# Kernel tuning notes

Measured on AMD Instinct MI355X. Metric: run time of the kernel, lower is better.

## Reference

```python
import jax, jax.numpy as jnp
import numpy as np

ALPHA = 0.2
N_NODES = 50000
N_REL = 500
E = 500000
E_NHOP = 100000


def l2norm(v):
    n = jnp.sqrt(jnp.sum(v * v, axis=1, keepdims=True))
    return v / jnp.maximum(n, 1e-12)


def sp_attention(x, src, dst, edge_embed, a, a2, concat):
    # a: [out, 2*din + drel]; edge_m = a @ cat(x[src], x[dst], edge_embed).T, done blockwise
    N, din = x.shape
    a_src, a_dst, a_rel = a[:, :din], a[:, din:2 * din], a[:, 2 * din:]
    edge_m = x[src] @ a_src.T + x[dst] @ a_dst.T + edge_embed @ a_rel.T  # [E, out]
    powers = -jax.nn.leaky_relu(edge_m @ a2, ALPHA)                      # [E]
    edge_e = jnp.exp(powers)
    e_rowsum = jax.ops.segment_sum(edge_e, src, num_segments=N)
    e_rowsum = jnp.where(e_rowsum == 0.0, 1e-12, e_rowsum)
    h_prime = jax.ops.segment_sum(edge_e[:, None] * edge_m, src, num_segments=N)
    h_prime = h_prime / e_rowsum[:, None]
    return jax.nn.elu(h_prime) if concat else h_prime


def spgat(x, rel, src, dst, edge_type, et_nhop, head_params, W, out_a, out_a2):
    ee = jnp.concatenate([rel[edge_type], rel[et_nhop[:, 0]] + rel[et_nhop[:, 1]]], axis=0)
    x = jnp.concatenate([sp_attention(x, src, dst, ee, a, a2, True) for a, a2 in head_params], axis=1)
    out_rel = rel @ W
    ee2 = jnp.concatenate([out_rel[edge_type], out_rel[et_nhop[:, 0]] + out_rel[et_nhop[:, 1]]], axis=0)
    x = jax.nn.elu(sp_attention(x, src, dst, ee2, out_a, out_a2, False))
    return x, out_rel


def forward_impl(entity_emb, relation_emb, W_entities,
                 g0_a0, g0_s0, g0_a1, g0_s1, g0_W, g0_oa, g0_os,
                 g1_a0, g1_s0, g1_W, g1_oa, g1_os,
                 edge_list, edge_type, train_indices_nhop, batch_inputs):
    ent = l2norm(entity_emb)
    rel = l2norm(relation_emb)
    # n-hop edges: (col3 -> col0), relation pair in cols 1,2
    src = jnp.concatenate([edge_list[0], train_indices_nhop[:, 3]])
    dst = jnp.concatenate([edge_list[1], train_indices_nhop[:, 0]])
    et_nhop = train_indices_nhop[:, 1:3]
    mask = jnp.zeros((ent.shape[0],), ent.dtype).at[batch_inputs[:, 2]].set(1.0)
    # layer 0 (2 heads)
    ent_up = ent @ W_entities
    rel_up = rel @ W_entities
    e_new, r_new = spgat(ent, rel, src, dst, edge_type, et_nhop,
                         [(g0_a0, g0_s0), (g0_a1, g0_s1)], g0_W, g0_oa, g0_os)
    ent = l2norm(ent_up + mask[:, None] * e_new)
    rel = l2norm(rel_up + r_new)
    # layer 1 (1 head, residual)
    e_new, r_new = spgat(ent, rel, src, dst, edge_type, et_nhop,
                         [(g1_a0, g1_s0)], g1_W, g1_oa, g1_os)
    ent = l2norm(ent + mask[:, None] * e_new)
    rel = l2norm(rel + r_new)
    return ent, rel


def setup_inputs() -> dict:
    key = jax.random.key(0)
    ks = jax.random.split(key, 20)
    s = 0.05
    inp = {
        "entity_emb": jax.random.normal(ks[0], (N_NODES, 100), jnp.float32),
        "relation_emb": jax.random.normal(ks[1], (N_REL, 100), jnp.float32),
        "W_entities": jax.random.normal(ks[2], (100, 200), jnp.float32) * s,
        "g0_a0": jax.random.normal(ks[3], (100, 300), jnp.float32) * s,
        "g0_s0": jax.random.normal(ks[4], (100,), jnp.float32) * s,
        "g0_a1": jax.random.normal(ks[5], (100, 300), jnp.float32) * s,
        "g0_s1": jax.random.normal(ks[6], (100,), jnp.float32) * s,
        "g0_W": jax.random.normal(ks[7], (100, 200), jnp.float32) * s,
        "g0_oa": jax.random.normal(ks[8], (200, 600), jnp.float32) * s,
        "g0_os": jax.random.normal(ks[9], (200,), jnp.float32) * s,
        "g1_a0": jax.random.normal(ks[10], (200, 600), jnp.float32) * s,
        "g1_s0": jax.random.normal(ks[11], (200,), jnp.float32) * s,
        "g1_W": jax.random.normal(ks[12], (200, 200), jnp.float32) * s,
        "g1_oa": jax.random.normal(ks[13], (200, 600), jnp.float32) * s,
        "g1_os": jax.random.normal(ks[14], (200,), jnp.float32) * s,
        "edge_list": jax.random.randint(ks[15], (2, E), 0, N_NODES, jnp.int64 if jax.config.jax_enable_x64 else jnp.int32),
        "edge_type": jax.random.randint(ks[16], (E,), 0, N_REL),
        "train_indices_nhop": jax.random.randint(ks[17], (E_NHOP, 4), 0, N_REL),
        "batch_inputs": jax.random.randint(ks[18], (10000, 3), 0, N_NODES),
    }
    return inp


def reference(entity_emb, relation_emb, W_entities,
              g0_a0, g0_s0, g0_a1, g0_s1, g0_W, g0_oa, g0_os,
              g1_a0, g1_s0, g1_W, g1_oa, g1_os,
              edge_list, edge_type, train_indices_nhop, batch_inputs):
    return forward_impl(entity_emb, relation_emb, W_entities,
                        g0_a0, g0_s0, g0_a1, g0_s1, g0_W, g0_oa, g0_os,
                        g1_a0, g1_s0, g1_W, g1_oa, g1_os,
                        edge_list, edge_type, train_indices_nhop, batch_inputs)
```

## Files before the change

kernel.cpp:

```cpp
#include <hip/hip_runtime.h>
#include <hip/hip_bf16.h>
#include <cstdint>
#include <cstddef>

#define NNODES 50000
#define NRELS  500
#define NEDGE  500000
#define NETOT  600000
#define MP     50048
#define RPAD   512
#define HOTN   512

typedef __attribute__((ext_vector_type(8))) short bf16x8;
typedef __attribute__((ext_vector_type(4))) float f32x4;

__device__ inline float bf2f(unsigned short s){
  union { unsigned u; float f; } v; v.u = ((unsigned)s) << 16; return v.f;
}
__device__ inline unsigned short f2bf(float f){
  __hip_bfloat16 h = __float2bfloat16(f);
  return __builtin_bit_cast(unsigned short, h);
}

struct WEnt { int src, ld, boff, rows, K, tr, dstoff, Kp, rp; };
// ... 94 lines not shown

__global__ void k_mask_set(const int* __restrict__ batch, float* __restrict__ mask, int nb){
  int i = blockIdx.x*blockDim.x + threadIdx.x;
  if (i < nb) mask[batch[3*i+2]] = 1.0f;
}

__global__ void k_hist(const int* __restrict__ el, const int* __restrict__ nh, int* __restrict__ deg){
  int e = blockIdx.x*blockDim.x + threadIdx.x;
  if (e >= NETOT) return;
  int s = (e < NEDGE) ? el[e] : nh[4*(e-NEDGE)+3];
  atomicAdd(&deg[s], 1);
}
__global__ void k_scan1(int* __restrict__ data, int n, int* __restrict__ part){
  __shared__ int sh[256];
  int t = threadIdx.x, i = blockIdx.x*256 + t;
  int v = (i < n) ? data[i] : 0;
  sh[t] = v; __syncthreads();
  for (int o = 1; o < 256; o <<= 1){
    int x = (t >= o) ? sh[t-o] : 0;
    __syncthreads(); sh[t] += x; __syncthreads();
  }
  if (i < n) data[i] = sh[t] - v;
  if (t == 255) part[blockIdx.x] = sh[255];
}
__global__ void k_scan2(int* __restrict__ part, int nb){
  __shared__ int sh[256];
  int t = threadIdx.x;
  int v = (t < nb) ? part[t] : 0;
  sh[t] = v; __syncthreads();
  for (int o = 1; o < 256; o <<= 1){
    int x = (t >= o) ? sh[t-o] : 0;
    __syncthreads(); sh[t] += x; __syncthreads();
  }
  if (t < nb) part[t] = sh[t] - v;
}
__global__ void k_scan3(int* __restrict__ data, int n, const int* __restrict__ part){
  int i = blockIdx.x*256 + threadIdx.x;
  if (i < n) data[i] += part[blockIdx.x];
  if (i == 0) data[n] = NETOT;
}
__global__ void k_scatter(const int* __restrict__ el, const int* __restrict__ et,
                          const int* __restrict__ nh, const int* __restrict__ rowofs,
                          int* __restrict__ cur, int4* __restrict__ erec){
  int e = blockIdx.x*blockDim.x + threadIdx.x;
  if (e >= NETOT) return;
  int s, d, t0, t1;
  if (e < NEDGE){ s = el[e]; d = el[NEDGE+e]; t0 = et[e]; t1 = NRELS; }
  else { int i = e - NEDGE; s = nh[4*i+3]; d = nh[4*i+0]; t0 = nh[4*i+1]; t1 = nh[4*i+2]; }
  int p = rowofs[s] + atomicAdd(&cur[s], 1);
  erec[p] = make_int4(d, t0, t1, 0);
}

template<bool FINAL>
__global__ __launch_bounds__(64) void k_combine2(
    const __hip_bfloat16* __restrict__ baseE, const __hip_bfloat16* __restrict__ hE,
    const float* __restrict__ mask,
    const __hip_bfloat16* __restrict__ baseR, const __hip_bfloat16* __restrict__ hR,
    float* __restrict__ outfE, float* __restrict__ outfR,
    __hip_bfloat16* __restrict__ outbE, __hip_bfloat16* __restrict__ outbR)
{
  int n = blockIdx.x, lane = threadIdx.x;
  bool isE = n < NNODES;
  int row = isE ? n : n - NNODES;
  const __hip_bfloat16* b = (isE ? baseE : baseR) + (size_t)row*224;
  const __hip_bfloat16* h = (isE ? hE : hR) + (size_t)row*224;
  float m = isE ? mask[row] : 1.0f;
  int c = lane*4;
  float4 v = make_float4(0.f,0.f,0.f,0.f);
  if (c < 200){
    ushort4 bb = *(const ushort4*)(b + c);
    ushort4 hh = *(const ushort4*)(h + c);
    v.x = bf2f(bb.x) + m*bf2f(hh.x);
    v.y = bf2f(bb.y) + m*bf2f(hh.y);
    v.z = bf2f(bb.z) + m*bf2f(hh.z);
    v.w = bf2f(bb.w) + m*bf2f(hh.w);
  }
  float ss = v.x*v.x + v.y*v.y + v.z*v.z + v.w*v.w;
  #pragma unroll
  for (int o = 32; o; o >>= 1) ss += __shfl_xor(ss, o, 64);
  float sc = 1.0f / fmaxf(sqrtf(ss), 1e-12f);
  if constexpr (FINAL){
    if (c < 200){
      float* o = (isE ? outfE : outfR) + (size_t)row*200 + c;
      *(float4*)o = make_float4(v.x*sc, v.y*sc, v.z*sc, v.w*sc);
    }
  } else {
    if (c < 224){
      __hip_bfloat16* o = (isE ? outbE : outbR) + (size_t)row*224 + c;
      ushort4 w4; w4.x = f2bf(v.x*sc); w4.y = f2bf(v.y*sc); w4.z = f2bf(v.z*sc); w4.w = f2bf(v.w*sc);
      *(ushort4*)o = w4;
    }
  }
}

__global__ __launch_bounds__(256) void k_rowdot3(
    const __hip_bfloat16* __restrict__ XN, const float* __restrict__ wtN, int GN,
    float* __restrict__ n0, float* __restrict__ n1, float* __restrict__ n2, float* __restrict__ n3,
    const __hip_bfloat16* __restrict__ XR, const float* __restrict__ wtR, int GR,
    float* __restrict__ r0, float* __restrict__ r1)
{
  int wave = threadIdx.x >> 6, lane = threadIdx.x & 63;
  int b = blockIdx.x;
  if (b < 12500){
    int row = b*4 + wave;
    const __hip_bfloat16* xr = XN + (size_t)row*512 + lane*8;
    const float* wr = wtN + lane*8;
    float p = 0.f;
    #pragma unroll
    for (int k = 0; k < 2; k++){
      ushort4 x = *(const ushort4*)(xr + 4*k);
      float4 a = *(const float4*)(wr + 4*k);
      p += bf2f(x.x)*a.x + bf2f(x.y)*a.y + bf2f(x.z)*a.z + bf2f(x.w)*a.w;
    }
    for (int o = GN>>1; o; o >>= 1) p += __shfl_xor(p, o, 64);
    if ((lane & (GN-1)) == 0){
      int g = lane / GN;
      float* out = (g==0)?n0:(g==1)?n1:(g==2)?n2:n3;
      out[row] = p;
    }
  } else {
    int row = (b - 12500)*4 + wave;
    if (row >= NRELS + 1) return;
    const __hip_bfloat16* xr = XR + (size_t)row*256 + lane*4;
    ushort4 x = *(const ushort4*)xr;
    float4 a = *(const float4*)(wtR + lane*4);
    float p = bf2f(x.x)*a.x + bf2f(x.y)*a.y + bf2f(x.z)*a.z + bf2f(x.w)*a.w;
    for (int o = GR>>1; o; o >>= 1) p += __shfl_xor(p, o, 64);
    if ((lane & (GR-1)) == 0){
      int g = lane / GR;
      float* out = (g==0)?r0:r1;
      out[row] = p;
    }
  }
}

struct GemmDesc {
  const __hip_bfloat16 *A, *B; __hip_bfloat16* C;
  int M, Nn, Kp, ldc, gx, nblk;
};
__global__ __launch_bounds__(256) void k_gemm2(GemmDesc g1, GemmDesc g2)
{
  __shared__ __hip_bfloat16 As[128*32];
  __shared__ __hip_bfloat16 Bs[64*32];
// ... 23 lines not shown

  for (int kk = 0; kk < Kp; kk += 32){
    {
      int p0 = ap ^ ((ar0 >> 1) & 3);
      const char* s0 = Ab + ((size_t)(m0 + ar0)*Kp + kk)*2 + p0*16;
      __builtin_amdgcn_global_load_lds((const __attribute__((address_space(1))) void*)s0,
          (__attribute__((address_space(3))) void*)(asB + wave*1024), 16, 0, 0);
      int p1 = ap ^ ((ar1 >> 1) & 3);
      const char* s1 = Ab + ((size_t)(m0 + ar1)*Kp + kk)*2 + p1*16;
      __builtin_amdgcn_global_load_lds((const __attribute__((address_space(1))) void*)s1,
          (__attribute__((address_space(3))) void*)(asB + 4096 + wave*1024), 16, 0, 0);
      int pb = ap ^ ((ar0 >> 1) & 3);
      const char* sb = Bb + ((size_t)(n0 + ar0)*Kp + kk)*2 + pb*16;
      __builtin_amdgcn_global_load_lds((const __attribute__((address_space(1))) void*)sb,
          (__attribute__((address_space(3))) void*)(bsB + wave*1024), 16, 0, 0);
    }
    __syncthreads();
    bf16x8 av[4], bv[2];
    #pragma unroll
    for (int mf = 0; mf < 4; mf++){
      int row = wr*64 + mf*16 + li;
      int p = lg ^ ((row >> 1) & 3);
      av[mf] = *(const bf16x8*)(asB + row*64 + p*16);
    }
    #pragma unroll
    for (int nf = 0; nf < 2; nf++){
      int row = wc*32 + nf*16 + li;
      int p = lg ^ ((row >> 1) & 3);
      bv[nf] = *(const bf16x8*)(bsB + row*64 + p*16);
    }
    #pragma unroll
    for (int mf = 0; mf < 4; mf++)
      #pragma unroll
      for (int nf = 0; nf < 2; nf++)
        acc[mf][nf] = __builtin_amdgcn_mfma_f32_16x16x32_bf16(av[mf], bv[nf], acc[mf][nf], 0, 0, 0);
    __syncthreads();
  }
  #pragma unroll
  for (int mf = 0; mf < 4; mf++){
    #pragma unroll
    for (int nf = 0; nf < 2; nf++){
      int gc = n0 + wc*32 + nf*16 + li;
      if (gc >= g.Nn) continue;
      int gr0 = m0 + wr*64 + mf*16 + lg*4;
      #pragma unroll
      for (int rr = 0; rr < 4; rr++){
        int gr = gr0 + rr;
        if (gr < g.M) g.C[(size_t)gr*g.ldc + gc] = __float2bfloat16(acc[mf][nf][rr]);
      }
    }
  }
}

__device__ inline void agg5_edges(int bstart, int end, int bstep,
    const int4* __restrict__ erec, float psn,
    const float* __restrict__ pd, const float* __restrict__ prs,
    const __hip_bfloat16* __restrict__ XSD, int ldx, int cxd,
    const __hip_bfloat16* __restrict__ RRb, int ldr, int crr,
    int lane, float& Sl, float4& accO)
{
  bool act = lane < 50;
  const __hip_bfloat16* xb = XSD + cxd + 4*lane;
  const __hip_bfloat16* rb = RRb + crr + 4*lane;
  float4 accA = make_float4(0.f,0.f,0.f,0.f);
  float4 accB = make_float4(0.f,0.f,0.f,0.f);
  for (int b = bstart; b < end; b += bstep){
    int j = b + lane;
    int4 e = make_int4(0, NRELS, NRELS, 0);
    float wv = 0.f;
    if (j < end){
      e = erec[j];
      float lg = psn + pd[e.x] + prs[e.y] + prs[e.z];
      wv = __expf(-((lg > 0.f) ? lg : 0.2f*lg));
    }
    Sl += wv;
    int m = end - b; if (m > 64) m = 64;
    int i = 0;
    for (; i + 1 < m; i += 2){
      float wA = __shfl(wv, i),   wB = __shfl(wv, i+1);
      int dA = __shfl(e.x, i),   tA0 = __shfl(e.y, i),   tA1 = __shfl(e.z, i);
      int dB = __shfl(e.x, i+1), tB0 = __shfl(e.y, i+1), tB1 = __shfl(e.z, i+1);
      if (act){
        ushort4 xA = *(const ushort4*)(xb + (size_t)dA*ldx);
        ushort4 rA = *(const ushort4*)(rb + (size_t)tA0*ldr);
        ushort4 xB = *(const ushort4*)(xb + (size_t)dB*ldx);
        ushort4 rB = *(const ushort4*)(rb + (size_t)tB0*ldr);
        float ax = bf2f(xA.x)+bf2f(rA.x), ay = bf2f(xA.y)+bf2f(rA.y);
        float az = bf2f(xA.z)+bf2f(rA.z), aw = bf2f(xA.w)+bf2f(rA.w);
        if (tA1 != NRELS){
          ushort4 rc = *(const ushort4*)(rb + (size_t)tA1*ldr);
          ax += bf2f(rc.x); ay += bf2f(rc.y); az += bf2f(rc.z); aw += bf2f(rc.w);
        }
        float bx = bf2f(xB.x)+bf2f(rB.x), by = bf2f(xB.y)+bf2f(rB.y);
        float bz = bf2f(xB.z)+bf2f(rB.z), bw = bf2f(xB.w)+bf2f(rB.w);
        if (tB1 != NRELS){
          ushort4 rc = *(const ushort4*)(rb + (size_t)tB1*ldr);
          bx += bf2f(rc.x); by += bf2f(rc.y); bz += bf2f(rc.z); bw += bf2f(rc.w);
        }
        accA.x += wA*ax; accA.y += wA*ay; accA.z += wA*az; accA.w += wA*aw;
        accB.x += wB*bx; accB.y += wB*by; accB.z += wB*bz; accB.w += wB*bw;
      }
    }
    if (i < m){
      float wA = __shfl(wv, i);
      int dA = __shfl(e.x, i), tA0 = __shfl(e.y, i), tA1 = __shfl(e.z, i);
      if (act){
        ushort4 xA = *(const ushort4*)(xb + (size_t)dA*ldx);
        ushort4 rA = *(const ushort4*)(rb + (size_t)tA0*ldr);
        float ax = bf2f(xA.x)+bf2f(rA.x), ay = bf2f(xA.y)+bf2f(rA.y);
        float az = bf2f(xA.z)+bf2f(rA.z), aw = bf2f(xA.w)+bf2f(rA.w);
        if (tA1 != NRELS){
          ushort4 rc = *(const ushort4*)(rb + (size_t)tA1*ldr);
          ax += bf2f(rc.x); ay += bf2f(rc.y); az += bf2f(rc.z); aw += bf2f(rc.w);
        }
        accA.x += wA*ax; accA.y += wA*ay; accA.z += wA*az; accA.w += wA*aw;
      }
    }
  }
  accO.x += accA.x + accB.x; accO.y += accA.y + accB.y;
  accO.z += accA.z + accB.z; accO.w += accA.w + accB.w;
}

__device__ inline void agg5_finalize(int n, float S, float4 acc, int lane,
    const __hip_bfloat16* __restrict__ XSD, int ldx, int cxs,
    __hip_bfloat16* __restrict__ outb, int ldb, int coffb)
{
  if (lane >= 50) return;
  float inv = (S > 0.f) ? 1.0f/S : 0.f;
  ushort4 xs4 = *(const ushort4*)(XSD + (size_t)n*ldx + cxs + 4*lane);
  float h0 = (S > 0.f) ? bf2f(xs4.x) + acc.x*inv : 0.f;
  float h1 = (S > 0.f) ? bf2f(xs4.y) + acc.y*inv : 0.f;
  float h2 = (S > 0.f) ? bf2f(xs4.z) + acc.z*inv : 0.f;
  float h3 = (S > 0.f) ? bf2f(xs4.w) + acc.w*inv : 0.f;
  h0 = (h0 > 0.f) ? h0 : expm1f(h0);
  h1 = (h1 > 0.f) ? h1 : expm1f(h1);
  h2 = (h2 > 0.f) ? h2 : expm1f(h2);
  h3 = (h3 > 0.f) ? h3 : expm1f(h3);
  ushort4 o; o.x = f2bf(h0); o.y = f2bf(h1); o.z = f2bf(h2); o.w = f2bf(h3);
  *(ushort4*)(outb + (size_t)n*ldb + coffb + 4*lane) = o;
}

__global__ __launch_bounds__(256) void k_agg5(
    const int* __restrict__ rowofs, const int4* __restrict__ erec,
    const float* __restrict__ ps, const float* __restrict__ pd, const float* __restrict__ prs,
    const __hip_bfloat16* __restrict__ XSD,
    const __hip_bfloat16* __restrict__ RRb,
    __hip_bfloat16* __restrict__ outb, int ldb, int coffb)
{
  __shared__ float4 redA[256];
  __shared__ float redS[4];
  int bid = blockIdx.x;
  int wave = threadIdx.x >> 6, lane = threadIdx.x & 63;

  if (bid < HOTN){
    int n = bid;
    int beg = rowofs[n], end = rowofs[n+1];
    float psn = ps[n];
    float Sl = 0.f;
    float4 acc = make_float4(0.f,0.f,0.f,0.f);
    agg5_edges(beg + wave*64, end, 256, erec, psn, pd, prs,
               XSD, 512, 256, RRb, 256, 0, lane, Sl, acc);
    float Sw = Sl;
    #pragma unroll
    for (int o = 32; o; o >>= 1) Sw += __shfl_xor(Sw, o, 64);
    redA[threadIdx.x] = acc;
    if (lane == 0) redS[wave] = Sw;
    __syncthreads();
    if (wave == 0){
      float4 a0 = redA[lane], a1 = redA[lane+64], a2 = redA[lane+128], a3 = redA[lane+192];
      float4 at = make_float4(a0.x+a1.x+a2.x+a3.x, a0.y+a1.y+a2.y+a3.y,
                              a0.z+a1.z+a2.z+a3.z, a0.w+a1.w+a2.w+a3.w);
      float St = redS[0] + redS[1] + redS[2] + redS[3];
      agg5_finalize(n, St, at, lane, XSD, 512, 0, outb, ldb, coffb);
    }
  } else {
    int n = HOTN + (bid - HOTN)*4 + wave;
    int beg = rowofs[n], end = rowofs[n+1];
    float psn = ps[n];
    float Sl = 0.f;
    float4 acc = make_float4(0.f,0.f,0.f,0.f);
    agg5_edges(beg, end, 64, erec, psn, pd, prs,
               XSD, 512, 256, RRb, 256, 0, lane, Sl, acc);
    float S = Sl;
    #pragma unroll
    for (int o = 32; o; o >>= 1) S += __shfl_xor(S, o, 64);
    agg5_finalize(n, S, acc, lane, XSD, 512, 0, outb, ldb, coffb);
  }
}

__device__ inline void aggh_edges(int bstart, int end, int bstep,
    const int4* __restrict__ erec,
    float ps0n, const float* __restrict__ pd0, const float* __restrict__ prs0,
    float ps1n, const float* __restrict__ pd1, const float* __restrict__ prs1,
    const __hip_bfloat16* __restrict__ XSD, int ldx,
    const __hip_bfloat16* __restrict__ RRb, int ldr,
    int lane, float& Sl0, float& Sl1, float4& accO)
{
  bool act = lane < 50;
  int head = (lane >= 25) ? 1 : 0;
  int li = lane - 25*head;
  const __hip_bfloat16* xb = XSD + (head ? 384 : 128) + 4*li;
  const __hip_bfloat16* rb = RRb + (head ? 128 : 0) + 4*li;
  float4 accA = make_float4(0.f,0.f,0.f,0.f);
  float4 accB = make_float4(0.f,0.f,0.f,0.f);
  for (int b = bstart; b < end; b += bstep){
    int j = b + lane;
    int4 e = make_int4(0, NRELS, NRELS, 0);
    float wv0 = 0.f, wv1 = 0.f;
    if (j < end){
      e = erec[j];
      float lg0 = ps0n + pd0[e.x] + prs0[e.y] + prs0[e.z];
      float lg1 = ps1n + pd1[e.x] + prs1[e.y] + prs1[e.z];
      wv0 = __expf(-((lg0 > 0.f) ? lg0 : 0.2f*lg0));
      wv1 = __expf(-((lg1 > 0.f) ? lg1 : 0.2f*lg1));
    }
    Sl0 += wv0; Sl1 += wv1;
    int m = end - b; if (m > 64) m = 64;
    int i = 0;
    for (; i + 1 < m; i += 2){
      float wA0 = __shfl(wv0, i),   wA1 = __shfl(wv1, i);
      float wB0 = __shfl(wv0, i+1), wB1 = __shfl(wv1, i+1);
      int dA = __shfl(e.x, i),   tA0 = __shfl(e.y, i),   tA1 = __shfl(e.z, i);
      int dB = __shfl(e.x, i+1), tB0 = __shfl(e.y, i+1), tB1 = __shfl(e.z, i+1);
      if (act){
        float wA = head ? wA1 : wA0;
        float wB = head ? wB1 : wB0;
        ushort4 xA = *(const ushort4*)(xb + (size_t)dA*ldx);
        ushort4 rA = *(const ushort4*)(rb + (size_t)tA0*ldr);
        ushort4 xB = *(const ushort4*)(xb + (size_t)dB*ldx);
        ushort4 rB = *(const ushort4*)(rb + (size_t)tB0*ldr);
        float ax = bf2f(xA.x)+bf2f(rA.x), ay = bf2f(xA.y)+bf2f(rA.y);
        float az = bf2f(xA.z)+bf2f(rA.z), aw = bf2f(xA.w)+bf2f(rA.w);
        if (tA1 != NRELS){
          ushort4 rc = *(const ushort4*)(rb + (size_t)tA1*ldr);
          ax += bf2f(rc.x); ay += bf2f(rc.y); az += bf2f(rc.z); aw += bf2f(rc.w);
        }
        float bx = bf2f(xB.x)+bf2f(rB.x), by = bf2f(xB.y)+bf2f(rB.y);
        float bz = bf2f(xB.z)+bf2f(rB.z), bw = bf2f(xB.w)+bf2f(rB.w);
        if (tB1 != NRELS){
          ushort4 rc = *(const ushort4*)(rb + (size_t)tB1*ldr);
          bx += bf2f(rc.x); by += bf2f(rc.y); bz += bf2f(rc.z); bw += bf2f(rc.w);
        }
        accA.x += wA*ax; accA.y += wA*ay; accA.z += wA*az; accA.w += wA*aw;
        accB.x += wB*bx; accB.y += wB*by; accB.z += wB*bz; accB.w += wB*bw;
      }
    }
    if (i < m){
      float wA0 = __shfl(wv0, i), wA1 = __shfl(wv1, i);
      int dA = __shfl(e.x, i), tA0 = __shfl(e.y, i), tA1 = __shfl(e.z, i);
      if (act){
        float wA = head ? wA1 : wA0;
        ushort4 xA = *(const ushort4*)(xb + (size_t)dA*ldx);
        ushort4 rA = *(const ushort4*)(rb + (size_t)tA0*ldr);
        float ax = bf2f(xA.x)+bf2f(rA.x), ay = bf2f(xA.y)+bf2f(rA.y);
        float az = bf2f(xA.z)+bf2f(rA.z), aw = bf2f(xA.w)+bf2f(rA.w);
        if (tA1 != NRELS){
          ushort4 rc = *(const ushort4*)(rb + (size_t)tA1*ldr);
          ax += bf2f(rc.x); ay += bf2f(rc.y); az += bf2f(rc.z); aw += bf2f(rc.w);
        }
        accA.x += wA*ax; accA.y += wA*ay; accA.z += wA*az; accA.w += wA*aw;
      }
    }
  }
  accO.x += accA.x + accB.x; accO.y += accA.y + accB.y;
  accO.z += accA.z + accB.z; accO.w += accA.w + accB.w;
}

__device__ inline void aggh_finalize(int n, float S0, float S1, float4 acc, int lane,
    const __hip_bfloat16* __restrict__ XSD,
    __hip_bfloat16* __restrict__ outb, int ldb)
{
  if (lane >= 50) return;
  int head = (lane >= 25) ? 1 : 0;
  int li = lane - 25*head;
  float S = head ? S1 : S0;
  float inv = (S > 0.f) ? 1.0f/S : 0.f;
  ushort4 xs4 = *(const ushort4*)(XSD + (size_t)n*512 + (head ? 256 : 0) + 4*li);
  float h0 = (S > 0.f) ? bf2f(xs4.x) + acc.x*inv : 0.f;
  float h1 = (S > 0.f) ? bf2f(xs4.y) + acc.y*inv : 0.f;
  float h2 = (S > 0.f) ? bf2f(xs4.z) + acc.z*inv : 0.f;
  float h3 = (S > 0.f) ? bf2f(xs4.w) + acc.w*inv : 0.f;
  h0 = (h0 > 0.f) ? h0 : expm1f(h0);
  h1 = (h1 > 0.f) ? h1 : expm1f(h1);
  h2 = (h2 > 0.f) ? h2 : expm1f(h2);
  h3 = (h3 > 0.f) ? h3 : expm1f(h3);
  ushort4 o; o.x = f2bf(h0); o.y = f2bf(h1); o.z = f2bf(h2); o.w = f2bf(h3);
  *(ushort4*)(outb + (size_t)n*ldb + 100*head + 4*li) = o;
}

__global__ __launch_bounds__(256) void k_aggh(
    const int* __restrict__ rowofs, const int4* __restrict__ erec,
    const float* __restrict__ ps0, const float* __restrict__ pd0, const float* __restrict__ prs0,
    const float* __restrict__ ps1, const float* __restrict__ pd1, const float* __restrict__ prs1,
    const __hip_bfloat16* __restrict__ XSD, const __hip_bfloat16* __restrict__ RRb,
    __hip_bfloat16* __restrict__ outb, int ldb)
{
  __shared__ float4 redA[256];
  __shared__ float redS0[4];
  __shared__ float redS1[4];
  int bid = blockIdx.x;
  int wave = threadIdx.x >> 6, lane = threadIdx.x & 63;

  if (bid < HOTN){
    int n = bid;
    int beg = rowofs[n], end = rowofs[n+1];
    float ps0n = ps0[n], ps1n = ps1[n];
    float Sl0 = 0.f, Sl1 = 0.f;
    float4 acc = make_float4(0.f,0.f,0.f,0.f);
    aggh_edges(beg + wave*64, end, 256, erec, ps0n, pd0, prs0, ps1n, pd1, prs1,
               XSD, 512, RRb, 256, lane, Sl0, Sl1, acc);
    float Sw0 = Sl0, Sw1 = Sl1;
    #pragma unroll
    for (int o = 32; o; o >>= 1){ Sw0 += __shfl_xor(Sw0, o, 64); Sw1 += __shfl_xor(Sw1, o, 64); }
    redA[threadIdx.x] = acc;
    if (lane == 0){ redS0[wave] = Sw0; redS1[wave] = Sw1; }
    __syncthreads();
    if (wave == 0){
      float4 a0 = redA[lane], a1 = redA[lane+64], a2 = redA[lane+128], a3 = redA[lane+192];
      float4 at = make_float4(a0.x+a1.x+a2.x+a3.x, a0.y+a1.y+a2.y+a3.y,
                              a0.z+a1.z+a2.z+a3.z, a0.w+a1.w+a2.w+a3.w);
      float St0 = redS0[0] + redS0[1] + redS0[2] + redS0[3];
      float St1 = redS1[0] + redS1[1] + redS1[2] + redS1[3];
      aggh_finalize(n, St0, St1, at, lane, XSD, outb, ldb);
    }
  } else {
    int n = HOTN + (bid - HOTN)*4 + wave;
    int beg = rowofs[n], end = rowofs[n+1];
    float ps0n = ps0[n], ps1n = ps1[n];
    float Sl0 = 0.f, Sl1 = 0.f;
    float4 acc = make_float4(0.f,0.f,0.f,0.f);
    aggh_edges(beg, end, 64, erec, ps0n, pd0, prs0, ps1n, pd1, prs1,
               XSD, 512, RRb, 256, lane, Sl0, Sl1, acc);
    float S0 = Sl0, S1 = Sl1;
    #pragma unroll
    for (int o = 32; o; o >>= 1){ S0 += __shfl_xor(S0, o, 64); S1 += __shfl_xor(S1, o, 64); }
    aggh_finalize(n, S0, S1, acc, lane, XSD, outb, ldb);
  }
}

extern "C" void kernel_launch(void* const* d_in, const int* in_sizes, int n_in,
                              void* d_out, int out_size, void* d_ws, size_t ws_size,
                              hipStream_t stream) {
  const float* entity   = (const float*)d_in[0];
  const float* relation = (const float*)d_in[1];
  const float* W_ent    = (const float*)d_in[2];
  const float* g0_a0    = (const float*)d_in[3];
  const float* g0_s0    = (const float*)d_in[4];
  const float* g0_a1    = (const float*)d_in[5];
  const float* g0_s1    = (const float*)d_in[6];
  const float* g0_W     = (const float*)d_in[7];
  const float* g0_oa    = (const float*)d_in[8];
  const float* g0_os    = (const float*)d_in[9];
  const float* g1_a0    = (const float*)d_in[10];
  const float* g1_s0    = (const float*)d_in[11];
  const float* g1_W     = (const float*)d_in[12];
  const float* g1_oa    = (const float*)d_in[13];
  const float* g1_os    = (const float*)d_in[14];
  const int*   el       = (const int*)d_in[15];
  const int*   et       = (const int*)d_in[16];
  const int*   nh       = (const int*)d_in[17];
  const int*   batch    = (const int*)d_in[18];
  (void)in_sizes; (void)n_in; (void)out_size; (void)ws_size;

  char* w = (char*)d_ws;
  auto alloc = [&](size_t bytes)->char*{ char* p = w; w += (bytes + 255) & ~(size_t)255; return p; };
  float* PS0   = (float*)alloc((size_t)NNODES*4);
  float* PD0   = (float*)alloc((size_t)NNODES*4);
  float* PS1   = (float*)alloc((size_t)NNODES*4);
  float* PD1   = (float*)alloc((size_t)NNODES*4);
  float* PRS0  = (float*)alloc((size_t)(NRELS+4)*4);
  float* PRS1  = (float*)alloc((size_t)(NRELS+4)*4);
  float* WT    = (float*)alloc((size_t)2304*4);
  __hip_bfloat16* AENT0  = (__hip_bfloat16*)alloc((size_t)MP*128*2);
  __hip_bfloat16* AX1    = (__hip_bfloat16*)alloc((size_t)MP*224*2);
  __hip_bfloat16* AENT1  = (__hip_bfloat16*)alloc((size_t)MP*224*2);
  __hip_bfloat16* ENTUPb = (__hip_bfloat16*)alloc((size_t)MP*224*2);
  __hip_bfloat16* HB     = (__hip_bfloat16*)alloc((size_t)MP*224*2);
  __hip_bfloat16* AREL0  = (__hip_bfloat16*)alloc((size_t)RPAD*128*2);
  __hip_bfloat16* AREL1  = (__hip_bfloat16*)alloc((size_t)RPAD*224*2);
  __hip_bfloat16* RELUPb = (__hip_bfloat16*)alloc((size_t)RPAD*224*2);
  __hip_bfloat16* ORb0   = (__hip_bfloat16*)alloc((size_t)RPAD*224*2);
  __hip_bfloat16* ORb1   = (__hip_bfloat16*)alloc((size_t)RPAD*224*2);
  __hip_bfloat16* XSD    = (__hip_bfloat16*)alloc((size_t)MP*512*2);
  __hip_bfloat16* RRb    = (__hip_bfloat16*)alloc((size_t)RPAD*256*2);
  __hip_bfloat16* WA     = (__hip_bfloat16*)alloc((size_t)737280*2);
  int* IALL = (int*)alloc((size_t)150001*4);
  int* ROWOFS = IALL;
  int* CUR    = IALL + 50001;
  float* MASK = (float*)(IALL + 100001);
  int4* EREC  = (int4*)alloc((size_t)NETOT*16);
  int* PART   = (int*)alloc((size_t)256*4);

  const __hip_bfloat16* WET   = WA;
  const __hip_bfloat16* G0WT  = WA + 32768;
  const __hip_bfloat16* BH0   = WA + 65536;
  const __hip_bfloat16* BR0   = WA + 131072;
  const __hip_bfloat16* BO0   = WA + 163840;
  const __hip_bfloat16* BO0r  = WA + 278528;
  const __hip_bfloat16* BA1   = WA + 335872;
  const __hip_bfloat16* BA1r  = WA + 450560;
  const __hip_bfloat16* G1WT  = WA + 507904;
  const __hip_bfloat16* BO1   = WA + 565248;
  const __hip_bfloat16* BO1r  = WA + 679936;

  float* outEnt = (float*)d_out;
  float* outRel = outEnt + (size_t)NNODES*200;

  const int TB = 256;
  auto gb = [&](long long n){ return (int)((n + TB - 1)/TB); };
  const int AGG_GRID = HOTN + (NNODES - HOTN)/4;
  const int RD_GRID = 12500 + 126;

  {
    SetupArgs a;
    a.iall = IALL; a.aent0 = AENT0; a.ax1 = AX1; a.aent1 = AENT1; a.arel0 = AREL0; a.arel1 = AREL1;
    a.wt = WT; a.s0h = g0_s0; a.s1h = g0_s1; a.os0 = g0_os; a.s1l = g1_s0; a.os1 = g1_os;
    a.wa = WA;
    a.wsrcs.p[0] = W_ent; a.wsrcs.p[1] = g0_a0; a.wsrcs.p[2] = g0_a1; a.wsrcs.p[3] = g0_W;
    a.wsrcs.p[4] = g0_oa; a.wsrcs.p[5] = g1_a0; a.wsrcs.p[6] = g1_W;  a.wsrcs.p[7] = g1_oa;
    a.entity = entity; a.relation = relation;
    k_setup<<<SB_TOT, 256, 0, stream>>>(a);
  }
  k_mask_set<<<gb(10000), TB, 0, stream>>>(batch, MASK, 10000);
  k_hist<<<gb(NETOT), TB, 0, stream>>>(el, nh, ROWOFS);
  int nsb = (NNODES + 255)/256;
  k_scan1<<<nsb, 256, 0, stream>>>(ROWOFS, NNODES, PART);
  k_scan2<<<1, 256, 0, stream>>>(PART, nsb);
  k_scan3<<<nsb, 256, 0, stream>>>(ROWOFS, NNODES, PART);
  k_scatter<<<gb(NETOT), TB, 0, stream>>>(el, et, nh, ROWOFS, CUR, EREC);

  auto mkdesc = [](const __hip_bfloat16* A, const __hip_bfloat16* B, __hip_bfloat16* C,
                   int M, int Nn, int Kp, int ldc){
    GemmDesc d; d.A = A; d.B = B; d.C = C; d.M = M; d.Nn = Nn; d.Kp = Kp; d.ldc = ldc;
    d.gx = (Nn + 63)/64; d.nblk = d.gx * ((M + 127)/128); return d;
  };
  GemmDesc dnull = {}; dnull.nblk = 0;
  auto gemm2 = [&](GemmDesc d1, GemmDesc d2){
    k_gemm2<<<d1.nblk + d2.nblk, 256, 0, stream>>>(d1, d2);
  };

  gemm2(mkdesc(AENT0, WET, ENTUPb, MP, 200, 128, 224),
        mkdesc(AREL0, WET, RELUPb, RPAD, 200, 128, 224));

  gemm2(mkdesc(AENT0, BH0, XSD, MP, 512, 128, 512),
        mkdesc(AREL0, BR0, RRb, RPAD, 256, 128, 256));
  k_rowdot3<<<RD_GRID, 256, 0, stream>>>(XSD, WT + 0, 16, PS0, PD0, PS1, PD1,
                                         RRb, WT + 512, 32, PRS0, PRS1);
  k_aggh<<<AGG_GRID, 256, 0, stream>>>(ROWOFS, EREC, PS0, PD0, PRS0, PS1, PD1, PRS1,
                                       XSD, RRb, AX1, 224);

  gemm2(mkdesc(AX1, BO0, XSD, MP, 512, 224, 512),
        mkdesc(AREL0, G0WT, ORb0, RPAD, 224, 128, 224));
  gemm2(mkdesc(ORb0, BO0r, RRb, RPAD, 256, 224, 256), dnull);
  k_rowdot3<<<RD_GRID, 256, 0, stream>>>(XSD, WT + 768, 32, PS0, PD0, nullptr, nullptr,
                                         RRb, WT + 768, 64, PRS0, nullptr);
  k_agg5<<<AGG_GRID, 256, 0, stream>>>(ROWOFS, EREC, PS0, PD0, PRS0, XSD, RRb, HB, 224, 0);
  k_combine2<false><<<NNODES + NRELS, 64, 0, stream>>>(ENTUPb, HB, MASK, RELUPb, ORb0,
      nullptr, nullptr, AENT1, AREL1);

  gemm2(mkdesc(AENT1, BA1, XSD, MP, 512, 224, 512),
        mkdesc(AREL1, BA1r, RRb, RPAD, 256, 224, 256));
  k_rowdot3<<<RD_GRID, 256, 0, stream>>>(XSD, WT + 1280, 32, PS0, PD0, nullptr, nullptr,
                                         RRb, WT + 1280, 64, PRS0, nullptr);
  k_agg5<<<AGG_GRID, 256, 0, stream>>>(ROWOFS, EREC, PS0, PD0, PRS0, XSD, RRb, AX1, 224, 0);

  gemm2(mkdesc(AX1, BO1, XSD, MP, 512, 224, 512),
        mkdesc(AREL1, G1WT, ORb1, RPAD, 224, 224, 224));
  gemm2(mkdesc(ORb1, BO1r, RRb, RPAD, 256, 224, 256), dnull);
  k_rowdot3<<<RD_GRID, 256, 0, stream>>>(XSD, WT + 1792, 32, PS0, PD0, nullptr, nullptr,
                                         RRb, WT + 1792, 64, PRS0, nullptr);
  k_agg5<<<AGG_GRID, 256, 0, stream>>>(ROWOFS, EREC, PS0, PD0, PRS0, XSD, RRb, HB, 224, 0);

  k_combine2<true><<<NNODES + NRELS, 64, 0, stream>>>(AENT1, HB, MASK, AREL1, ORb1,
      outEnt, outRel, nullptr, nullptr);
}
```

Before: 580.4 us.

## Fuse residual combine and L2 norm into aggregation finalize; unroll edge loop by four

Entity rows now get the masked residual add, L2 normalisation and output write inside the k_agg5 finalize (templated by mode), so the HB intermediate buffer and a 50k-block combine kernel are gone. Only relations still use a small separate combine kernel. The edge gather loops in k_agg5 and k_aggh are unrolled from two to four edges with four independent accumulators, putting more gathers in flight. The cost is higher register pressure and slightly different float summation order.

```diff
diff --git a/kernel.cpp b/kernel.cpp
--- a/kernel.cpp
+++ b/kernel.cpp
@@ -170,43 +170,31 @@
 }
 
 template<bool FINAL>
-__global__ __launch_bounds__(64) void k_combine2(
-    const __hip_bfloat16* __restrict__ baseE, const __hip_bfloat16* __restrict__ hE,
-    const float* __restrict__ mask,
-    const __hip_bfloat16* __restrict__ baseR, const __hip_bfloat16* __restrict__ hR,
-    float* __restrict__ outfE, float* __restrict__ outfR,
-    __hip_bfloat16* __restrict__ outbE, __hip_bfloat16* __restrict__ outbR)
-{
-  int n = blockIdx.x, lane = threadIdx.x;
-  bool isE = n < NNODES;
-  int row = isE ? n : n - NNODES;
-  const __hip_bfloat16* b = (isE ? baseE : baseR) + (size_t)row*224;
-  const __hip_bfloat16* h = (isE ? hE : hR) + (size_t)row*224;
-  float m = isE ? mask[row] : 1.0f;
+__global__ __launch_bounds__(64) void k_combine_rel(
+    const __hip_bfloat16* __restrict__ base, const __hip_bfloat16* __restrict__ h,
+    float* __restrict__ outf, __hip_bfloat16* __restrict__ outb)
+{
+  int row = blockIdx.x, lane = threadIdx.x;
   int c = lane*4;
   float4 v = make_float4(0.f,0.f,0.f,0.f);
   if (c < 200){
-    ushort4 bb = *(const ushort4*)(b + c);
-    ushort4 hh = *(const ushort4*)(h + c);
-    v.x = bf2f(bb.x) + m*bf2f(hh.x);
-    v.y = bf2f(bb.y) + m*bf2f(hh.y);
-    v.z = bf2f(bb.z) + m*bf2f(hh.z);
-    v.w = bf2f(bb.w) + m*bf2f(hh.w);
+    ushort4 bb = *(const ushort4*)(base + (size_t)row*224 + c);
+    ushort4 hh = *(const ushort4*)(h + (size_t)row*224 + c);
+    v.x = bf2f(bb.x) + bf2f(hh.x);
+    v.y = bf2f(bb.y) + bf2f(hh.y);
+    v.z = bf2f(bb.z) + bf2f(hh.z);
+    v.w = bf2f(bb.w) + bf2f(hh.w);
   }
   float ss = v.x*v.x + v.y*v.y + v.z*v.z + v.w*v.w;
   #pragma unroll
   for (int o = 32; o; o >>= 1) ss += __shfl_xor(ss, o, 64);
   float sc = 1.0f / fmaxf(sqrtf(ss), 1e-12f);
   if constexpr (FINAL){
-    if (c < 200){
-      float* o = (isE ? outfE : outfR) + (size_t)row*200 + c;
-      *(float4*)o = make_float4(v.x*sc, v.y*sc, v.z*sc, v.w*sc);
-    }
+    if (c < 200) *(float4*)(outf + (size_t)row*200 + c) = make_float4(v.x*sc, v.y*sc, v.z*sc, v.w*sc);
   } else {
     if (c < 224){
-      __hip_bfloat16* o = (isE ? outbE : outbR) + (size_t)row*224 + c;
       ushort4 w4; w4.x = f2bf(v.x*sc); w4.y = f2bf(v.y*sc); w4.z = f2bf(v.z*sc); w4.w = f2bf(v.w*sc);
-      *(ushort4*)o = w4;
+      *(ushort4*)(outb + (size_t)row*224 + c) = w4;
     }
   }
 }
@@ -336,6 +324,19 @@
   }
 }
 
+#define EDGE_LOAD(W, D, T0, T1, OUTX, OUTY, OUTZ, OUTW)                       \
+  {                                                                           \
+    ushort4 xq = *(const ushort4*)(xb + (size_t)(D)*ldx);                     \
+    ushort4 rq = *(const ushort4*)(rb + (size_t)(T0)*ldr);                    \
+    float qx = bf2f(xq.x)+bf2f(rq.x), qy = bf2f(xq.y)+bf2f(rq.y);             \
+    float qz = bf2f(xq.z)+bf2f(rq.z), qw = bf2f(xq.w)+bf2f(rq.w);             \
+    if ((T1) != NRELS){                                                       \
+      ushort4 rc = *(const ushort4*)(rb + (size_t)(T1)*ldr);                  \
+      qx += bf2f(rc.x); qy += bf2f(rc.y); qz += bf2f(rc.z); qw += bf2f(rc.w); \
+    }                                                                         \
+    OUTX += (W)*qx; OUTY += (W)*qy; OUTZ += (W)*qz; OUTW += (W)*qw;           \
+  }
+
 __device__ inline void agg5_edges(int bstart, int end, int bstep,
     const int4* __restrict__ erec, float psn,
     const float* __restrict__ pd, const float* __restrict__ prs,
@@ -346,8 +347,10 @@
   bool act = lane < 50;
   const __hip_bfloat16* xb = XSD + cxd + 4*lane;
   const __hip_bfloat16* rb = RRb + crr + 4*lane;
-  float4 accA = make_float4(0.f,0.f,0.f,0.f);
-  float4 accB = make_float4(0.f,0.f,0.f,0.f);
+  float4 a0 = make_float4(0.f,0.f,0.f,0.f);
+  float4 a1 = make_float4(0.f,0.f,0.f,0.f);
+  float4 a2 = make_float4(0.f,0.f,0.f,0.f);
+  float4 a3 = make_float4(0.f,0.f,0.f,0.f);
   for (int b = bstart; b < end; b += bstep){
     int j = b + lane;
     int4 e = make_int4(0, NRELS, NRELS, 0);
@@ -360,76 +363,92 @@
     Sl += wv;
     int m = end - b; if (m > 64) m = 64;
     int i = 0;
-    for (; i + 1 < m; i += 2){
-      float wA = __shfl(wv, i),   wB = __shfl(wv, i+1);
-      int dA = __shfl(e.x, i),   tA0 = __shfl(e.y, i),   tA1 = __shfl(e.z, i);
-      int dB = __shfl(e.x, i+1), tB0 = __shfl(e.y, i+1), tB1 = __shfl(e.z, i+1);
+    for (; i + 3 < m; i += 4){
+      float w0 = __shfl(wv, i),   w1 = __shfl(wv, i+1);
+      float w2 = __shfl(wv, i+2), w3 = __shfl(wv, i+3);
+      int d0 = __shfl(e.x, i),   u0 = __shfl(e.y, i),   v0 = __shfl(e.z, i);
+      int d1 = __shfl(e.x, i+1), u1 = __shfl(e.y, i+1), v1 = __shfl(e.z, i+1);
+      int d2 = __shfl(e.x, i+2), u2 = __shfl(e.y, i+2), v2 = __shfl(e.z, i+2);
+      int d3 = __shfl(e.x, i+3), u3 = __shfl(e.y, i+3), v3 = __shfl(e.z, i+3);
       if (act){
-        ushort4 xA = *(const ushort4*)(xb + (size_t)dA*ldx);
-        ushort4 rA = *(const ushort4*)(rb + (size_t)tA0*ldr);
-        ushort4 xB = *(const ushort4*)(xb + (size_t)dB*ldx);
-        ushort4 rB = *(const ushort4*)(rb + (size_t)tB0*ldr);
-        float ax = bf2f(xA.x)+bf2f(rA.x), ay = bf2f(xA.y)+bf2f(rA.y);
-        float az = bf2f(xA.z)+bf2f(rA.z), aw = bf2f(xA.w)+bf2f(rA.w);
-        if (tA1 != NRELS){
-          ushort4 rc = *(const ushort4*)(rb + (size_t)tA1*ldr);
-          ax += bf2f(rc.x); ay += bf2f(rc.y); az += bf2f(rc.z); aw += bf2f(rc.w);
-        }
-        float bx = bf2f(xB.x)+bf2f(rB.x), by = bf2f(xB.y)+bf2f(rB.y);
-        float bz = bf2f(xB.z)+bf2f(rB.z), bw = bf2f(xB.w)+bf2f(rB.w);
-        if (tB1 != NRELS){
-          ushort4 rc = *(const ushort4*)(rb + (size_t)tB1*ldr);
-          bx += bf2f(rc.x); by += bf2f(rc.y); bz += bf2f(rc.z); bw += bf2f(rc.w);
-        }
-        accA.x += wA*ax; accA.y += wA*ay; accA.z += wA*az; accA.w += wA*aw;
-        accB.x += wB*bx; accB.y += wB*by; accB.z += wB*bz; accB.w += wB*bw;
+        EDGE_LOAD(w0, d0, u0, v0, a0.x, a0.y, a0.z, a0.w)
+        EDGE_LOAD(w1, d1, u1, v1, a1.x, a1.y, a1.z, a1.w)
+        EDGE_LOAD(w2, d2, u2, v2, a2.x, a2.y, a2.z, a2.w)
+        EDGE_LOAD(w3, d3, u3, v3, a3.x, a3.y, a3.z, a3.w)
       }
     }
-    if (i < m){
-      float wA = __shfl(wv, i);
-      int dA = __shfl(e.x, i), tA0 = __shfl(e.y, i), tA1 = __shfl(e.z, i);
+    for (; i < m; ++i){
+      float w0 = __shfl(wv, i);
+      int d0 = __shfl(e.x, i), u0 = __shfl(e.y, i), v0 = __shfl(e.z, i);
       if (act){
-        ushort4 xA = *(const ushort4*)(xb + (size_t)dA*ldx);
-        ushort4 rA = *(const ushort4*)(rb + (size_t)tA0*ldr);
-        float ax = bf2f(xA.x)+bf2f(rA.x), ay = bf2f(xA.y)+bf2f(rA.y);
-        float az = bf2f(xA.z)+bf2f(rA.z), aw = bf2f(xA.w)+bf2f(rA.w);
-        if (tA1 != NRELS){
-          ushort4 rc = *(const ushort4*)(rb + (size_t)tA1*ldr);
-          ax += bf2f(rc.x); ay += bf2f(rc.y); az += bf2f(rc.z); aw += bf2f(rc.w);
-        }
-        accA.x += wA*ax; accA.y += wA*ay; accA.z += wA*az; accA.w += wA*aw;
+        EDGE_LOAD(w0, d0, u0, v0, a0.x, a0.y, a0.z, a0.w)
       }
     }
   }
-  accO.x += accA.x + accB.x; accO.y += accA.y + accB.y;
-  accO.z += accA.z + accB.z; accO.w += accA.w + accB.w;
-}
-
+  accO.x += (a0.x + a1.x) + (a2.x + a3.x);
+  accO.y += (a0.y + a1.y) + (a2.y + a3.y);
+  accO.z += (a0.z + a1.z) + (a2.z + a3.z);
+  accO.w += (a0.w + a1.w) + (a2.w + a3.w);
+}
+
+template<int MODE>
 __device__ inline void agg5_finalize(int n, float S, float4 acc, int lane,
     const __hip_bfloat16* __restrict__ XSD, int ldx, int cxs,
-    __hip_bfloat16* __restrict__ outb, int ldb, int coffb)
-{
-  if (lane >= 50) return;
-  float inv = (S > 0.f) ? 1.0f/S : 0.f;
-  ushort4 xs4 = *(const ushort4*)(XSD + (size_t)n*ldx + cxs + 4*lane);
-  float h0 = (S > 0.f) ? bf2f(xs4.x) + acc.x*inv : 0.f;
-  float h1 = (S > 0.f) ? bf2f(xs4.y) + acc.y*inv : 0.f;
-  float h2 = (S > 0.f) ? bf2f(xs4.z) + acc.z*inv : 0.f;
-  float h3 = (S > 0.f) ? bf2f(xs4.w) + acc.w*inv : 0.f;
-  h0 = (h0 > 0.f) ? h0 : expm1f(h0);
-  h1 = (h1 > 0.f) ? h1 : expm1f(h1);
-  h2 = (h2 > 0.f) ? h2 : expm1f(h2);
-  h3 = (h3 > 0.f) ? h3 : expm1f(h3);
-  ushort4 o; o.x = f2bf(h0); o.y = f2bf(h1); o.z = f2bf(h2); o.w = f2bf(h3);
-  *(ushort4*)(outb + (size_t)n*ldb + coffb + 4*lane) = o;
-}
-
+    const __hip_bfloat16* __restrict__ baseb, const float* __restrict__ mask,
+    __hip_bfloat16* __restrict__ outb, int ldb, int coffb, float* __restrict__ outf)
+{
+  float4 h = make_float4(0.f,0.f,0.f,0.f);
+  if (lane < 50){
+    float inv = (S > 0.f) ? 1.0f/S : 0.f;
+    ushort4 xs4 = *(const ushort4*)(XSD + (size_t)n*ldx + cxs + 4*lane);
+    float h0 = (S > 0.f) ? bf2f(xs4.x) + acc.x*inv : 0.f;
+    float h1 = (S > 0.f) ? bf2f(xs4.y) + acc.y*inv : 0.f;
+    float h2 = (S > 0.f) ? bf2f(xs4.z) + acc.z*inv : 0.f;
+    float h3 = (S > 0.f) ? bf2f(xs4.w) + acc.w*inv : 0.f;
+    h.x = (h0 > 0.f) ? h0 : expm1f(h0);
+    h.y = (h1 > 0.f) ? h1 : expm1f(h1);
+    h.z = (h2 > 0.f) ? h2 : expm1f(h2);
+    h.w = (h3 > 0.f) ? h3 : expm1f(h3);
+  }
+  if constexpr (MODE == 0){
+    if (lane < 50){
+      ushort4 o; o.x = f2bf(h.x); o.y = f2bf(h.y); o.z = f2bf(h.z); o.w = f2bf(h.w);
+      *(ushort4*)(outb + (size_t)n*ldb + coffb + 4*lane) = o;
+    }
+  } else {
+    float m = mask[n];
+    float4 v = make_float4(0.f,0.f,0.f,0.f);
+    if (lane < 50){
+      ushort4 bb = *(const ushort4*)(baseb + (size_t)n*224 + 4*lane);
+      v.x = bf2f(bb.x) + m*h.x;
+      v.y = bf2f(bb.y) + m*h.y;
+      v.z = bf2f(bb.z) + m*h.z;
+      v.w = bf2f(bb.w) + m*h.w;
+    }
+    float ss = v.x*v.x + v.y*v.y + v.z*v.z + v.w*v.w;
+    #pragma unroll
+    for (int o = 32; o; o >>= 1) ss += __shfl_xor(ss, o, 64);
+    float sc = 1.0f / fmaxf(sqrtf(ss), 1e-12f);
+    if constexpr (MODE == 1){
+      if (lane < 56){
+        ushort4 o; o.x = f2bf(v.x*sc); o.y = f2bf(v.y*sc); o.z = f2bf(v.z*sc); o.w = f2bf(v.w*sc);
+        *(ushort4*)(outb + (size_t)n*224 + 4*lane) = o;
+      }
+    } else {
+      if (lane < 50)
+        *(float4*)(outf + (size_t)n*200 + 4*lane) = make_float4(v.x*sc, v.y*sc, v.z*sc, v.w*sc);
+    }
+  }
+}
+
+template<int MODE>
 __global__ __launch_bounds__(256) void k_agg5(
     const int* __restrict__ rowofs, const int4* __restrict__ erec,
     const float* __restrict__ ps, const float* __restrict__ pd, const float* __restrict__ prs,
     const __hip_bfloat16* __restrict__ XSD,
     const __hip_bfloat16* __restrict__ RRb,
-    __hip_bfloat16* __restrict__ outb, int ldb, int coffb)
+    const __hip_bfloat16* __restrict__ baseb, const float* __restrict__ mask,
+    __hip_bfloat16* __restrict__ outb, int ldb, int coffb, float* __restrict__ outf)
 {
   __shared__ float4 redA[256];
   __shared__ float redS[4];
@@ -451,11 +470,11 @@
     if (lane == 0) redS[wave] = Sw;
     __syncthreads();
     if (wave == 0){
-      float4 a0 = redA[lane], a1 = redA[lane+64], a2 = redA[lane+128], a3 = redA[lane+192];
-      float4 at = make_float4(a0.x+a1.x+a2.x+a3.x, a0.y+a1.y+a2.y+a3.y,
-                              a0.z+a1.z+a2.z+a3.z, a0.w+a1.w+a2.w+a3.w);
+      float4 q0 = redA[lane], q1 = redA[lane+64], q2 = redA[lane+128], q3 = redA[lane+192];
+      float4 at = make_float4(q0.x+q1.x+q2.x+q3.x, q0.y+q1.y+q2.y+q3.y,
+                              q0.z+q1.z+q2.z+q3.z, q0.w+q1.w+q2.w+q3.w);
       float St = redS[0] + redS[1] + redS[2] + redS[3];
-      agg5_finalize(n, St, at, lane, XSD, 512, 0, outb, ldb, coffb);
+      agg5_finalize<MODE>(n, St, at, lane, XSD, 512, 0, baseb, mask, outb, ldb, coffb, outf);
     }
   } else {
     int n = HOTN + (bid - HOTN)*4 + wave;
@@ -468,7 +487,7 @@
     float S = Sl;
     #pragma unroll
     for (int o = 32; o; o >>= 1) S += __shfl_xor(S, o, 64);
-    agg5_finalize(n, S, acc, lane, XSD, 512, 0, outb, ldb, coffb);
+    agg5_finalize<MODE>(n, S, acc, lane, XSD, 512, 0, baseb, mask, outb, ldb, coffb, outf);
   }
 }
 
@@ -485,8 +504,10 @@
   int li = lane - 25*head;
   const __hip_bfloat16* xb = XSD + (head ? 384 : 128) + 4*li;
   const __hip_bfloat16* rb = RRb + (head ? 128 : 0) + 4*li;
-  float4 accA = make_float4(0.f,0.f,0.f,0.f);
-  float4 accB = make_float4(0.f,0.f,0.f,0.f);
+  float4 a0 = make_float4(0.f,0.f,0.f,0.f);
+  float4 a1 = make_float4(0.f,0.f,0.f,0.f);
+  float4 a2 = make_float4(0.f,0.f,0.f,0.f);
+  float4 a3 = make_float4(0.f,0.f,0.f,0.f);
   for (int b = bstart; b < end; b += bstep){
     int j = b + lane;
     int4 e = make_int4(0, NRELS, NRELS, 0);
@@ -501,53 +522,39 @@
     Sl0 += wv0; Sl1 += wv1;
     int m = end - b; if (m > 64) m = 64;
     int i = 0;
-    for (; i + 1 < m; i += 2){
-      float wA0 = __shfl(wv0, i),   wA1 = __shfl(wv1, i);
-      float wB0 = __shfl(wv0, i+1), wB1 = __shfl(wv1, i+1);
-      int dA = __shfl(e.x, i),   tA0 = __shfl(e.y, i),   tA1 = __shfl(e.z, i);
-      int dB = __shfl(e.x, i+1), tB0 = __shfl(e.y, i+1), tB1 = __shfl(e.z, i+1);
+    for (; i + 3 < m; i += 4){
+      float wa0 = __shfl(wv0, i),   wa1 = __shfl(wv1, i);
+      float wb0 = __shfl(wv0, i+1), wb1 = __shfl(wv1, i+1);
+      float wc0 = __shfl(wv0, i+2), wc1 = __shfl(wv1, i+2);
+      float wd0 = __shfl(wv0, i+3), wd1 = __shfl(wv1, i+3);
+      int d0 = __shfl(e.x, i),   u0 = __shfl(e.y, i),   v0 = __shfl(e.z, i);
+      int d1 = __shfl(e.x, i+1), u1 = __shfl(e.y, i+1), v1 = __shfl(e.z, i+1);
+      int d2 = __shfl(e.x, i+2), u2 = __shfl(e.y, i+2), v2 = __shfl(e.z, i+2);
+      int d3 = __shfl(e.x, i+3), u3 = __shfl(e.y, i+3), v3 = __shfl(e.z, i+3);
       if (act){
-        float wA = head ? wA1 : wA0;
-        float wB = head ? wB1 : wB0;
-        ushort4 xA = *(const ushort4*)(xb + (size_t)dA*ldx);
-        ushort4 rA = *(const ushort4*)(rb + (size_t)tA0*ldr);
-        ushort4 xB = *(const ushort4*)(xb + (size_t)dB*ldx);
-        ushort4 rB = *(const ushort4*)(rb + (size_t)tB0*ldr);
-        float ax = bf2f(xA.x)+bf2f(rA.x), ay = bf2f(xA.y)+bf2f(rA.y);
-        float az = bf2f(xA.z)+bf2f(rA.z), aw = bf2f(xA.w)+bf2f(rA.w);
-        if (tA1 != NRELS){
-          ushort4 rc = *(const ushort4*)(rb + (size_t)tA1*ldr);
-          ax += bf2f(rc.x); ay += bf2f(rc.y); az += bf2f(rc.z); aw += bf2f(rc.w);
-        }
-        float bx = bf2f(xB.x)+bf2f(rB.x), by = bf2f(xB.y)+bf2f(rB.y);
-        float bz = bf2f(xB.z)+bf2f(rB.z), bw = bf2f(xB.w)+bf2f(rB.w);
-        if (tB1 != NRELS){
-          ushort4 rc = *(const ushort4*)(rb + (size_t)tB1*ldr);
-          bx += bf2f(rc.x); by += bf2f(rc.y); bz += bf2f(rc.z); bw += bf2f(rc.w);
-        }
-        accA.x += wA*ax; accA.y += wA*ay; accA.z += wA*az; accA.w += wA*aw;
-        accB.x += wB*bx; accB.y += wB*by; accB.z += wB*bz; accB.w += wB*bw;
+        float wA = head ? wa1 : wa0;
+        float wB = head ? wb1 : wb0;
+        float wC = head ? wc1 : wc0;
+        float wD = head ? wd1 : wd0;
+        EDGE_LOAD(wA, d0, u0, v0, a0.x, a0.y, a0.z, a0.w)
+        EDGE_LOAD(wB, d1, u1, v1, a1.x, a1.y, a1.z, a1.w)
+        EDGE_LOAD(wC, d2, u2, v2, a2.x, a2.y, a2.z, a2.w)
+        EDGE_LOAD(wD, d3, u3, v3, a3.x, a3.y, a3.z, a3.w)
       }
     }
-    if (i < m){
-      float wA0 = __shfl(wv0, i), wA1 = __shfl(wv1, i);
-      int dA = __shfl(e.x, i), tA0 = __shfl(e.y, i), tA1 = __shfl(e.z, i);
+    for (; i < m; ++i){
+      float wa0 = __shfl(wv0, i), wa1 = __shfl(wv1, i);
+      int d0 = __shfl(e.x, i), u0 = __shfl(e.y, i), v0 = __shfl(e.z, i);
       if (act){
-        float wA = head ? wA1 : wA0;
-        ushort4 xA = *(const ushort4*)(xb + (size_t)dA*ldx);
-        ushort4 rA = *(const ushort4*)(rb + (size_t)tA0*ldr);
-        float ax = bf2f(xA.x)+bf2f(rA.x), ay = bf2f(xA.y)+bf2f(rA.y);
-        float az = bf2f(xA.z)+bf2f(rA.z), aw = bf2f(xA.w)+bf2f(rA.w);
-        if (tA1 != NRELS){
-          ushort4 rc = *(const ushort4*)(rb + (size_t)tA1*ldr);
-          ax += bf2f(rc.x); ay += bf2f(rc.y); az += bf2f(rc.z); aw += bf2f(rc.w);
-        }
-        accA.x += wA*ax; accA.y += wA*ay; accA.z += wA*az; accA.w += wA*aw;
+        float wA = head ? wa1 : wa0;
+        EDGE_LOAD(wA, d0, u0, v0, a0.x, a0.y, a0.z, a0.w)
       }
     }
   }
-  accO.x += accA.x + accB.x; accO.y += accA.y + accB.y;
-  accO.z += accA.z + accB.z; accO.w += accA.w + accB.w;
+  accO.x += (a0.x + a1.x) + (a2.x + a3.x);
+  accO.y += (a0.y + a1.y) + (a2.y + a3.y);
+  accO.z += (a0.z + a1.z) + (a2.z + a3.z);
+  accO.w += (a0.w + a1.w) + (a2.w + a3.w);
 }
 
 __device__ inline void aggh_finalize(int n, float S0, float S1, float4 acc, int lane,
@@ -600,9 +607,9 @@
     if (lane == 0){ redS0[wave] = Sw0; redS1[wave] = Sw1; }
     __syncthreads();
     if (wave == 0){
-      float4 a0 = redA[lane], a1 = redA[lane+64], a2 = redA[lane+128], a3 = redA[lane+192];
-      float4 at = make_float4(a0.x+a1.x+a2.x+a3.x, a0.y+a1.y+a2.y+a3.y,
-                              a0.z+a1.z+a2.z+a3.z, a0.w+a1.w+a2.w+a3.w);
+      float4 q0 = redA[lane], q1 = redA[lane+64], q2 = redA[lane+128], q3 = redA[lane+192];
+      float4 at = make_float4(q0.x+q1.x+q2.x+q3.x, q0.y+q1.y+q2.y+q3.y,
+                              q0.z+q1.z+q2.z+q3.z, q0.w+q1.w+q2.w+q3.w);
       float St0 = redS0[0] + redS0[1] + redS0[2] + redS0[3];
       float St1 = redS1[0] + redS1[1] + redS1[2] + redS1[3];
       aggh_finalize(n, St0, St1, at, lane, XSD, outb, ldb);
@@ -659,7 +666,6 @@
   __hip_bfloat16* AX1    = (__hip_bfloat16*)alloc((size_t)MP*224*2);
   __hip_bfloat16* AENT1  = (__hip_bfloat16*)alloc((size_t)MP*224*2);
   __hip_bfloat16* ENTUPb = (__hip_bfloat16*)alloc((size_t)MP*224*2);
-  __hip_bfloat16* HB     = (__hip_bfloat16*)alloc((size_t)MP*224*2);
   __hip_bfloat16* AREL0  = (__hip_bfloat16*)alloc((size_t)RPAD*128*2);
   __hip_bfloat16* AREL1  = (__hip_bfloat16*)alloc((size_t)RPAD*224*2);
   __hip_bfloat16* RELUPb = (__hip_bfloat16*)alloc((size_t)RPAD*224*2);
@@ -738,23 +744,23 @@
   gemm2(mkdesc(ORb0, BO0r, RRb, RPAD, 256, 224, 256), dnull);
   k_rowdot3<<<RD_GRID, 256, 0, stream>>>(XSD, WT + 768, 32, PS0, PD0, nullptr, nullptr,
                                          RRb, WT + 768, 64, PRS0, nullptr);
-  k_agg5<<<AGG_GRID, 256, 0, stream>>>(ROWOFS, EREC, PS0, PD0, PRS0, XSD, RRb, HB, 224, 0);
-  k_combine2<false><<<NNODES + NRELS, 64, 0, stream>>>(ENTUPb, HB, MASK, RELUPb, ORb0,
-      nullptr, nullptr, AENT1, AREL1);
+  k_agg5<1><<<AGG_GRID, 256, 0, stream>>>(ROWOFS, EREC, PS0, PD0, PRS0, XSD, RRb,
+                                          ENTUPb, MASK, AENT1, 224, 0, nullptr);
+  k_combine_rel<false><<<NRELS, 64, 0, stream>>>(RELUPb, ORb0, nullptr, AREL1);
 
   gemm2(mkdesc(AENT1, BA1, XSD, MP, 512, 224, 512),
         mkdesc(AREL1, BA1r, RRb, RPAD, 256, 224, 256));
   k_rowdot3<<<RD_GRID, 256, 0, stream>>>(XSD, WT + 1280, 32, PS0, PD0, nullptr, nullptr,
                                          RRb, WT + 1280, 64, PRS0, nullptr);
-  k_agg5<<<AGG_GRID, 256, 0, stream>>>(ROWOFS, EREC, PS0, PD0, PRS0, XSD, RRb, AX1, 224, 0);
+  k_agg5<0><<<AGG_GRID, 256, 0, stream>>>(ROWOFS, EREC, PS0, PD0, PRS0, XSD, RRb,
+                                          nullptr, nullptr, AX1, 224, 0, nullptr);
 
   gemm2(mkdesc(AX1, BO1, XSD, MP, 512, 224, 512),
         mkdesc(AREL1, G1WT, ORb1, RPAD, 224, 224, 224));
   gemm2(mkdesc(ORb1, BO1r, RRb, RPAD, 256, 224, 256), dnull);
   k_rowdot3<<<RD_GRID, 256, 0, stream>>>(XSD, WT + 1792, 32, PS0, PD0, nullptr, nullptr,
                                          RRb, WT + 1792, 64, PRS0, nullptr);
-  k_agg5<<<AGG_GRID, 256, 0, stream>>>(ROWOFS, EREC, PS0, PD0, PRS0, XSD, RRb, HB, 224, 0);
-
-  k_combine2<true><<<NNODES + NRELS, 64, 0, stream>>>(AENT1, HB, MASK, AREL1, ORb1,
-      outEnt, outRel, nullptr, nullptr);
-}
+  k_agg5<2><<<AGG_GRID, 256, 0, stream>>>(ROWOFS, EREC, PS0, PD0, PRS0, XSD, RRb,
+                                          AENT1, MASK, nullptr, 0, 0, outEnt);
+  k_combine_rel<true><<<NRELS, 64, 0, stream>>>(AREL1, ORb1, outRel, nullptr);
+}
```

After: 668.9 us. 1.15x slower.
